# Performance work log

Hardware: AMD Instinct MI355X
Metric: run time of the kernel (lower is better)

The kernel has to match this reference:

```python
import jax, jax.numpy as jnp
import numpy as np

B, M, K, L, E = 1024, 16, 32, 50, 64
NUM_ACT, NUM_USER = 100000, 500000
AVG_M = float(M)  # avg group size; equals M since groups are batched to fixed size


def setup_inputs() -> dict:
    key = jax.random.key(0)
    ks = jax.random.split(key, 24)
    s = 1.0 / np.sqrt(E)
    u = lambda k, shape: jax.random.uniform(k, shape, minval=-s, maxval=s, dtype=jnp.float32)
    return {
        "members": jax.random.randint(ks[0], (B, M), 0, NUM_USER),
        "neighbors": jax.random.randint(ks[1], (B, M, K), 0, NUM_USER),
        "act_inputs": jax.random.randint(ks[2], (B,), 0, NUM_ACT),
        "act_seqs": jax.random.randint(ks[3], (B, M, L), 0, NUM_ACT),
        "act_table": jax.random.normal(ks[4], (NUM_ACT, E), dtype=jnp.float32) * 0.02,
        "user_table": jax.random.normal(ks[5], (NUM_USER, E), dtype=jnp.float32) * 0.02,
        "W_ih": u(ks[6], (4 * E, E)),
        "W_hh": u(ks[7], (4 * E, E)),
        "b_ih": u(ks[8], (4 * E,)),
        "b_hh": u(ks[9], (4 * E,)),
        "gcn_W": u(ks[10], (E, E)),
        "gcn_b": u(ks[11], (E,)),
        "pna_W1": u(ks[12], (4 * E, E)),
        "pna_b1": u(ks[13], (E,)),
        "pna_W2": u(ks[14], (E, E)),
        "pna_b2": u(ks[15], (E,)),
        "pna_W3": u(ks[16], (E, E)),
        "pna_b3": u(ks[17], (E,)),
        "pred_W1": u(ks[18], (3 * E, 8)),
        "pred_b1": u(ks[19], (8,)),
        "pred_W2": u(ks[20], (8, 1)),
        "pred_b2": u(ks[21], (1,)),
    }


def _lstm_last(x, W_ih, W_hh, b):
    # x: [N, L, E]; returns last hidden state [N, E] (PyTorch gate order i,f,g,o)
    n = x.shape[0]
    h0 = jnp.zeros((n, E), x.dtype)

    def step(carry, xt):
        h, c = carry
        gates = xt @ W_ih.T + h @ W_hh.T + b  # [N, 4E]
        i, f, g, o = jnp.split(gates, 4, axis=-1)
        c = jax.nn.sigmoid(f) * c + jax.nn.sigmoid(i) * jnp.tanh(g)
        h = jax.nn.sigmoid(o) * jnp.tanh(c)
        return (h, c), None

    (h, _), _ = jax.lax.scan(step, (h0, h0), jnp.swapaxes(x, 0, 1))
    return h


def reference(members, neighbors, act_inputs, act_seqs, act_table, user_table,
              W_ih, W_hh, b_ih, b_hh, gcn_W, gcn_b,
              pna_W1, pna_b1, pna_W2, pna_b2, pna_W3, pna_b3,
              pred_W1, pred_b1, pred_W2, pred_b2):
    act_e = act_table[act_inputs]  # [B, E] target activity embeddings
    # per-member LSTM encoding of activity sequences, batched over all B*M members
    seq_e = act_table[act_seqs].reshape(B * M, L, E)
    m_act = _lstm_last(seq_e, W_ih, W_hh, b_ih + b_hh).reshape(B, M, E)
    # GCN: mean over {member} U neighbors, then linear + relu
    mem_e = user_table[members]                     # [B, M, E]
    nbr_sum = user_table[neighbors].sum(axis=2)     # [B, M, E]
    agg = (mem_e + nbr_sum) / (K + 1)
    m_gcn = jax.nn.relu(agg @ gcn_W.T + gcn_b)      # [B, M, E]
    fus = m_act + m_gcn                             # [B, M, E]
    # PNA-style set aggregation: {mean,max} x {identity, amplification}
    mean = fus.mean(axis=1)
    mx = fus.max(axis=1)
    amp = jnp.log(M + 1.0) / jnp.log(AVG_M + 1.0)
    feats = jnp.concatenate([mean, mx, mean * amp, mx * amp], axis=-1)  # [B, 4E]
    h = jax.nn.relu(feats @ pna_W1 + pna_b1)
    h = jax.nn.relu(h @ pna_W2 + pna_b2)
    grp = h @ pna_W3 + pna_b3                        # [B, E]
    # predict layer
    cat = jnp.concatenate([grp * act_e, grp, act_e], axis=-1)  # [B, 3E]
    hh = jax.nn.relu(cat @ pred_W1 + pred_b1)
    y = jax.nn.sigmoid(hh @ pred_W2 + pred_b2)       # [B, 1]
    return y
```

## Files before the change

kernel.cpp:

```cpp
#include <hip/hip_runtime.h>
#include <hip/hip_bf16.h>
#include <math.h>

#define BB   1024
#define MM   16
#define KK   32
#define LL   50
#define EE   64
#define NACT 100000

typedef __attribute__((ext_vector_type(8))) short short8;
typedef float v4f __attribute__((ext_vector_type(4)));

__device__ __forceinline__ float rcpf(float x) { return __builtin_amdgcn_rcpf(x); }
__device__ __forceinline__ float exp2_fast(float x) {
    float r;
    asm("v_exp_f32 %0, %1" : "=v"(r) : "v"(x));
    return r;
}

__device__ __forceinline__ unsigned cvt_pk_bf16(float lo, float hi) {
    unsigned r;
    asm("v_cvt_pk_bf16_f32 %0, %1, %2" : "=v"(r) : "v"(lo), "v"(hi));
    return r;
}

__device__ __forceinline__ void block_sync_lds() {
    __builtin_amdgcn_sched_barrier(0);
    asm volatile("s_waitcnt lgkmcnt(0)" ::: "memory");
    __builtin_amdgcn_s_barrier();
    __builtin_amdgcn_sched_barrier(0);
}

__global__ __launch_bounds__(256)
void cvt_table(const float* __restrict__ src, unsigned* __restrict__ dst)
{
    const int i = blockIdx.x * 256 + threadIdx.x;
    if (i < (NACT * EE) / 8) {
        const float4* s = reinterpret_cast<const float4*>(src) + (size_t)i * 2;
        float4 a = s[0], b = s[1];
        uint4 o;
        o.x = cvt_pk_bf16(a.x, a.y);
        o.y = cvt_pk_bf16(a.z, a.w);
        o.z = cvt_pk_bf16(b.x, b.y);
        o.w = cvt_pk_bf16(b.z, b.w);
        reinterpret_cast<uint4*>(dst)[i] = o;
    }
}

__global__ __launch_bounds__(256, 2)
void lstm_fused(const int* __restrict__ act_seqs, const unsigned short* __restrict__ act_bf,
                const int* __restrict__ members, const int* __restrict__ neighbors,
                const float* __restrict__ user_table,
                const float* __restrict__ W_ih, const float* __restrict__ W_hh,
                const float* __restrict__ b_ih, const float* __restrict__ b_hh,
                const int* __restrict__ act_inputs, const float* __restrict__ act_table,
                const float* __restrict__ gcn_W, const float* __restrict__ gcn_b,
                const float* __restrict__ pna_W1, const float* __restrict__ pna_b1,
                const float* __restrict__ pna_W2, const float* __restrict__ pna_b2,
                const float* __restrict__ pna_W3, const float* __restrict__ pna_b3,
                const float* __restrict__ pred_W1, const float* __restrict__ pred_b1,
                const float* __restrict__ pred_W2, const float* __restrict__ pred_b2,
                float* __restrict__ out)
{
    __shared__ __align__(16) short sH[4][1024];
    __shared__ int sIdx[32 * LL];
    __shared__ int sNbr[32 * 33];
    __shared__ float sFus[32][66];
    __shared__ float sF[2][256];
    __shared__ float sP[2][2][64];
    __shared__ float sP7[2][8][8];
    __shared__ float sH1[2][64];
    __shared__ float sH2[2][64];
    __shared__ float sGrp[2][64];
    __shared__ float sActe[2][64];
    __shared__ float sHH[2][8];

    const int t    = threadIdx.x;
    const int blk  = blockIdx.x;
    const int lane = t & 63;
    const int w    = t >> 6;
    const int lr   = lane & 15;
    const int lb   = lane >> 4;

    for (int i = t; i < 32 * LL; i += 256) sIdx[i] = act_seqs[blk * (32 * LL) + i];
    for (int i = t; i < 32 * 33; i += 256) {
        const int p = i / 33, j = i - p * 33;
        const int base = blk * 32 + p;
        sNbr[i] = (j == 0) ? members[base] : neighbors[base * KK + j - 1];
    }
    if (t < 128) {
        const int q = t >> 6, e = t & 63;
        sActe[q][e] = act_table[(size_t)act_inputs[blk * 2 + q] * EE + e];
    }

    const float L2E = 1.44269504088896f;
    float gscale[4];
    gscale[0] = -L2E; gscale[1] = -L2E; gscale[2] = 2.0f * L2E; gscale[3] = -L2E;

    short8 Bf[2][4][2];
    #pragma unroll
    for (int mat = 0; mat < 2; ++mat) {
        const float* W = mat ? W_hh : W_ih;
        #pragma unroll
        for (int g = 0; g < 4; ++g) {
            const int j = g * 64 + w * 16 + lr;
            const float sc = gscale[g];
            #pragma unroll
            for (int ks = 0; ks < 2; ++ks) {
                const float4* p = reinterpret_cast<const float4*>(&W[(size_t)j * 64 + ks * 32 + lb * 8]);
                float4 v0 = p[0], v1 = p[1];
                uint4 o;
                o.x = cvt_pk_bf16(sc * v0.x, sc * v0.y);
                o.y = cvt_pk_bf16(sc * v0.z, sc * v0.w);
                o.z = cvt_pk_bf16(sc * v1.x, sc * v1.y);
                o.w = cvt_pk_bf16(sc * v1.z, sc * v1.w);
                Bf[mat][g][ks] = __builtin_bit_cast(short8, o);
            }
        }
    }
    short8 Bg[2];
    #pragma unroll
    for (int ks = 0; ks < 2; ++ks) {
        const int j = w * 16 + lr;
        const float4* p = reinterpret_cast<const float4*>(&gcn_W[(size_t)j * 64 + ks * 32 + lb * 8]);
        float4 v0 = p[0], v1 = p[1];
        uint4 o;
        o.x = cvt_pk_bf16(v0.x, v0.y);
        o.y = cvt_pk_bf16(v0.z, v0.w);
        o.z = cvt_pk_bf16(v1.x, v1.y);
        o.w = cvt_pk_bf16(v1.z, v1.w);
        Bg[ks] = __builtin_bit_cast(short8, o);
    }
    const float gb = gcn_b[w * 16 + lr];

    float bias[4];
    #pragma unroll
    for (int g = 0; g < 4; ++g) {
        const int j = g * 64 + w * 16 + lr;
        bias[g] = gscale[g] * (b_ih[j] + b_hh[j]);
    }

    float hA[4], cA[4], hB[4], cB[4];
    #pragma unroll
    for (int r = 0; r < 4; ++r) { hA[r] = 0.0f; cA[r] = 0.0f; hB[r] = 0.0f; cB[r] = 0.0f; }

    reinterpret_cast<uint4*>(sH)[t] = make_uint4(0u, 0u, 0u, 0u);
    __syncthreads();

    const int gpair = t >> 3;
    const int gec   = t & 7;
    const float* gut = user_table + (size_t)gec * 8;
    float gacc[8];
    #pragma unroll
    for (int q = 0; q < 8; ++q) gacc[q] = 0.0f;
    float4 gld0, gld1;
    {
        const int gi = sNbr[gpair * 33 + 0];
        const float4* gp = reinterpret_cast<const float4*>(gut + (size_t)gi * EE);
        gld0 = gp[0]; gld1 = gp[1];
    }

    const char* tbl8 = reinterpret_cast<const char*>(act_bf) + lb * 16;
    const int ibA = lr * LL;
    const int ibB = (16 + lr) * LL;

    int idA = sIdx[ibA + 0], idB = sIdx[ibB + 0];
    short8 axA0 = *reinterpret_cast<const short8*>(tbl8 + (size_t)idA * 128);
    short8 axA1 = *reinterpret_cast<const short8*>(tbl8 + (size_t)idA * 128 + 64);
    short8 axB0 = *reinterpret_cast<const short8*>(tbl8 + (size_t)idB * 128);
    short8 axB1 = *reinterpret_cast<const short8*>(tbl8 + (size_t)idB * 128 + 64);
    idA = sIdx[ibA + 1]; idB = sIdx[ibB + 1];

    const int offA0 = lr * 128 + ((lb ^ (lr & 7)) << 4);
    const int offA1 = lr * 128 + (((lb + 4) ^ (lr & 7)) << 4);
    int hw_off[4];
    #pragma unroll
    for (int r = 0; r < 4; ++r) {
        const int s = lb * 4 + r, e = w * 16 + lr;
        hw_off[r] = s * 128 + ((((e >> 3) ^ (s & 7)) << 4)) + (e & 7) * 2;
    }
    char* const sHb = reinterpret_cast<char*>(sH);

    #pragma unroll 2
    for (int step = 0; step < LL; ++step) {
        const int cb  = (step & 1) << 12;
        const int nb_ = cb ^ 4096;

        if (step < 33) {
            gacc[0] += gld0.x; gacc[1] += gld0.y; gacc[2] += gld0.z; gacc[3] += gld0.w;
            gacc[4] += gld1.x; gacc[5] += gld1.y; gacc[6] += gld1.z; gacc[7] += gld1.w;
            if (step < 32) {
                const int gi = sNbr[gpair * 33 + step + 1];
                const float4* gp = reinterpret_cast<const float4*>(gut + (size_t)gi * EE);
                gld0 = gp[0]; gld1 = gp[1];
            }
        }

        short8 nxA0 = *reinterpret_cast<const short8*>(tbl8 + (size_t)idA * 128);
        short8 nxA1 = *reinterpret_cast<const short8*>(tbl8 + (size_t)idA * 128 + 64);
        short8 nxB0 = *reinterpret_cast<const short8*>(tbl8 + (size_t)idB * 128);
        short8 nxB1 = *reinterpret_cast<const short8*>(tbl8 + (size_t)idB * 128 + 64);
        {
            const int s2 = (step + 2 < LL) ? (step + 2) : (LL - 1);
            idA = sIdx[ibA + s2]; idB = sIdx[ibB + s2];
        }

        short8 ahA0 = *reinterpret_cast<const short8*>(sHb + cb + offA0);
        short8 ahA1 = *reinterpret_cast<const short8*>(sHb + cb + offA1);
        short8 ahB0 = *reinterpret_cast<const short8*>(sHb + cb + 2048 + offA0);
        short8 ahB1 = *reinterpret_cast<const short8*>(sHb + cb + 2048 + offA1);

        v4f accA[4], accB[4];
        #pragma unroll
        for (int g = 0; g < 4; ++g) {
            v4f a; a[0] = bias[g]; a[1] = bias[g]; a[2] = bias[g]; a[3] = bias[g];
            accA[g] = a; accB[g] = a;
        }
        #pragma unroll
        for (int g = 0; g < 4; ++g) {
            accA[g] = __builtin_amdgcn_mfma_f32_16x16x32_bf16(axA0, Bf[0][g][0], accA[g], 0, 0, 0);
            accA[g] = __builtin_amdgcn_mfma_f32_16x16x32_bf16(axA1, Bf[0][g][1], accA[g], 0, 0, 0);
            accA[g] = __builtin_amdgcn_mfma_f32_16x16x32_bf16(ahA0, Bf[1][g][0], accA[g], 0, 0, 0);
            accA[g] = __builtin_amdgcn_mfma_f32_16x16x32_bf16(ahA1, Bf[1][g][1], accA[g], 0, 0, 0);
        }
        #pragma unroll
        for (int g = 0; g < 4; ++g) {
            accB[g] = __builtin_amdgcn_mfma_f32_16x16x32_bf16(axB0, Bf[0][g][0], accB[g], 0, 0, 0);
            accB[g] = __builtin_amdgcn_mfma_f32_16x16x32_bf16(axB1, Bf[0][g][1], accB[g], 0, 0, 0);
            accB[g] = __builtin_amdgcn_mfma_f32_16x16x32_bf16(ahB0, Bf[1][g][0], accB[g], 0, 0, 0);
            accB[g] = __builtin_amdgcn_mfma_f32_16x16x32_bf16(ahB1, Bf[1][g][1], accB[g], 0, 0, 0);
        }

        {
            char* SH = sHb + nb_;
            #pragma unroll
            for (int r = 0; r < 4; ++r) {
                const float si = rcpf(1.0f + exp2_fast(accA[0][r]));
                const float sf = rcpf(1.0f + exp2_fast(accA[1][r]));
                const float tg = fmaf(-2.0f, rcpf(1.0f + exp2_fast(accA[2][r])), 1.0f);
                const float so = rcpf(1.0f + exp2_fast(accA[3][r]));
                const float cc = fmaf(sf, cA[r], si * tg);
                cA[r] = cc;
                hA[r] = so * fmaf(-2.0f, rcpf(1.0f + exp2_fast(cc * (2.0f * L2E))), 1.0f);
            }
            const unsigned a01 = cvt_pk_bf16(hA[0], hA[1]);
            const unsigned a23 = cvt_pk_bf16(hA[2], hA[3]);
            *reinterpret_cast<short*>(SH + hw_off[0]) = (short)(a01 & 0xFFFF);
            *reinterpret_cast<short*>(SH + hw_off[1]) = (short)(a01 >> 16);
            *reinterpret_cast<short*>(SH + hw_off[2]) = (short)(a23 & 0xFFFF);
            *reinterpret_cast<short*>(SH + hw_off[3]) = (short)(a23 >> 16);
            SH += 2048;
            #pragma unroll
            for (int r = 0; r < 4; ++r) {
                const float si = rcpf(1.0f + exp2_fast(accB[0][r]));
                const float sf = rcpf(1.0f + exp2_fast(accB[1][r]));
                const float tg = fmaf(-2.0f, rcpf(1.0f + exp2_fast(accB[2][r])), 1.0f);
                const float so = rcpf(1.0f + exp2_fast(accB[3][r]));
                const float cc = fmaf(sf, cB[r], si * tg);
                cB[r] = cc;
                hB[r] = so * fmaf(-2.0f, rcpf(1.0f + exp2_fast(cc * (2.0f * L2E))), 1.0f);
            }
            const unsigned b01 = cvt_pk_bf16(hB[0], hB[1]);
            const unsigned b23 = cvt_pk_bf16(hB[2], hB[3]);
            *reinterpret_cast<short*>(SH + hw_off[0]) = (short)(b01 & 0xFFFF);
            *reinterpret_cast<short*>(SH + hw_off[1]) = (short)(b01 >> 16);
            *reinterpret_cast<short*>(SH + hw_off[2]) = (short)(b23 & 0xFFFF);
            *reinterpret_cast<short*>(SH + hw_off[3]) = (short)(b23 >> 16);
        }

        block_sync_lds();

        axA0 = nxA0; axA1 = nxA1; axB0 = nxB0; axB1 = nxB1;
    }


    {
        const float sc = 1.0f / 33.0f;
        uint4 pk;
        pk.x = cvt_pk_bf16(gacc[0] * sc, gacc[1] * sc);
        pk.y = cvt_pk_bf16(gacc[2] * sc, gacc[3] * sc);
        pk.z = cvt_pk_bf16(gacc[4] * sc, gacc[5] * sc);
        pk.w = cvt_pk_bf16(gacc[6] * sc, gacc[7] * sc);
        const int row = gpair & 15;
        const int off = ((gpair >> 4) << 11) + row * 128 + ((gec ^ (row & 7)) << 4);
        *reinterpret_cast<uint4*>(sHb + off) = pk;
    }
    __syncthreads();

    {
        short8 agA0 = *reinterpret_cast<const short8*>(sHb + offA0);
        short8 agA1 = *reinterpret_cast<const short8*>(sHb + offA1);
        short8 agB0 = *reinterpret_cast<const short8*>(sHb + 2048 + offA0);
        short8 agB1 = *reinterpret_cast<const short8*>(sHb + 2048 + offA1);
        v4f z4 = {0.0f, 0.0f, 0.0f, 0.0f};
        v4f gA = __builtin_amdgcn_mfma_f32_16x16x32_bf16(agA0, Bg[0], z4, 0, 0, 0);
        gA = __builtin_amdgcn_mfma_f32_16x16x32_bf16(agA1, Bg[1], gA, 0, 0, 0);
        v4f gB = __builtin_amdgcn_mfma_f32_16x16x32_bf16(agB0, Bg[0], z4, 0, 0, 0);
        gB = __builtin_amdgcn_mfma_f32_16x16x32_bf16(agB1, Bg[1], gB, 0, 0, 0);
        const int e = w * 16 + lr;
        #pragma unroll
        for (int r = 0; r < 4; ++r) {
            sFus[lb * 4 + r][e]      = hA[r] + fmaxf(gA[r] + gb, 0.0f);
            sFus[16 + lb * 4 + r][e] = hB[r] + fmaxf(gB[r] + gb, 0.0f);
        }
    }
    __syncthreads();

    if (t < 128) {
        const int q = t >> 6, e = t & 63;
        float mn = 0.0f, mx = -INFINITY;
        #pragma unroll
        for (int m = 0; m < MM; ++m) { float v = sFus[q * 16 + m][e]; mn += v; mx = fmaxf(mx, v); }
        mn *= (1.0f / 16.0f);
        sF[q][e] = mn; sF[q][64 + e] = mx; sF[q][128 + e] = mn; sF[q][192 + e] = mx;
    }
    __syncthreads();

    {
        const int q = t >> 7, kh = (t >> 6) & 1, j = t & 63;
        float p = 0.0f;
        const float* Wp = pna_W1 + (size_t)(kh * 128) * 64 + j;
        const float* fp = &sF[q][kh * 128];
        #pragma unroll 16
        for (int k = 0; k < 128; ++k) p = fmaf(fp[k], Wp[(size_t)k * 64], p);
        sP[q][kh][j] = p;
    }
    __syncthreads();
    if (t < 128) {
        const int q = t >> 6, j = t & 63;
        sH1[q][j] = fmaxf(pna_b1[j] + sP[q][0][j] + sP[q][1][j], 0.0f);
    }
    __syncthreads();

    {
        const int q = t >> 7, kh = (t >> 6) & 1, j = t & 63;
        float p = 0.0f;
        #pragma unroll
        for (int k = 0; k < 32; ++k)
            p = fmaf(sH1[q][kh * 32 + k], pna_W2[(size_t)(kh * 32 + k) * 64 + j], p);
        sP[q][kh][j] = p;
    }
    __syncthreads();
    if (t < 128) {
        const int q = t >> 6, j = t & 63;
        sH2[q][j] = fmaxf(pna_b2[j] + sP[q][0][j] + sP[q][1][j], 0.0f);
    }
    __syncthreads();

    {
        const int q = t >> 7, kh = (t >> 6) & 1, j = t & 63;
        float p = 0.0f;
        #pragma unroll
        for (int k = 0; k < 32; ++k)
            p = fmaf(sH2[q][kh * 32 + k], pna_W3[(size_t)(kh * 32 + k) * 64 + j], p);
        sP[q][kh][j] = p;
    }
    __syncthreads();
    if (t < 128) {
        const int q = t >> 6, j = t & 63;
        sGrp[q][j] = pna_b3[j] + sP[q][0][j] + sP[q][1][j];
    }
    __syncthreads();

    if (t < 128) {
        const int q = t >> 6, kg = (t >> 3) & 7, j = t & 7;
        float a = 0.0f;
        #pragma unroll
        for (int kk = 0; kk < 24; ++kk) {
            const int k = kg * 24 + kk;
            const float cv = (k < 64) ? sGrp[q][k] * sActe[q][k]
                                      : ((k < 128) ? sGrp[q][k - 64] : sActe[q][k - 128]);
            a = fmaf(cv, pred_W1[k * 8 + j], a);
        }
        sP7[q][kg][j] = a;
    }
    __syncthreads();
    if (t < 16) {
        const int q = t >> 3, j = t & 7;
        float a = pred_b1[j];
        #pragma unroll
        for (int kg = 0; kg < 8; ++kg) a += sP7[q][kg][j];
        sHH[q][j] = fmaxf(a, 0.0f);
    }
    __syncthreads();
    if (t < 2) {
        float y = pred_b2[0];
        #pragma unroll
        for (int jj = 0; jj < 8; ++jj) y = fmaf(sHH[t][jj], pred_W2[jj], y);
        out[blk * 2 + t] = 1.0f / (1.0f + expf(-y));
    }
}

extern "C" void kernel_launch(void* const* d_in, const int* in_sizes, int n_in,
                              void* d_out, int out_size, void* d_ws, size_t ws_size,
                              hipStream_t stream) {
    const int*   members    = (const int*)d_in[0];
    const int*   neighbors  = (const int*)d_in[1];
    const int*   act_inputs = (const int*)d_in[2];
    const int*   act_seqs   = (const int*)d_in[3];
    const float* act_table  = (const float*)d_in[4];
    const float* user_table = (const float*)d_in[5];
    const float* W_ih       = (const float*)d_in[6];
    const float* W_hh       = (const float*)d_in[7];
    const float* b_ih       = (const float*)d_in[8];
    const float* b_hh       = (const float*)d_in[9];
    const float* gcn_W      = (const float*)d_in[10];
    const float* gcn_b      = (const float*)d_in[11];
    const float* pna_W1     = (const float*)d_in[12];
    const float* pna_b1     = (const float*)d_in[13];
    const float* pna_W2     = (const float*)d_in[14];
    const float* pna_b2     = (const float*)d_in[15];
    const float* pna_W3     = (const float*)d_in[16];
    const float* pna_b3     = (const float*)d_in[17];
    const float* pred_W1    = (const float*)d_in[18];
    const float* pred_b1    = (const float*)d_in[19];
    const float* pred_W2    = (const float*)d_in[20];
    const float* pred_b2    = (const float*)d_in[21];

    unsigned short* act_bf = (unsigned short*)d_ws;

    cvt_table<<<dim3((NACT * EE / 8 + 255) / 256), dim3(256), 0, stream>>>(
        act_table, (unsigned*)act_bf);

    lstm_fused<<<dim3(512), dim3(256), 0, stream>>>(
        act_seqs, act_bf, members, neighbors, user_table,
        W_ih, W_hh, b_ih, b_hh,
        act_inputs, act_table,
        gcn_W, gcn_b, pna_W1, pna_b1, pna_W2, pna_b2, pna_W3, pna_b3,
        pred_W1, pred_b1, pred_W2, pred_b2, (float*)d_out);
}
```

Baseline: 106.0 us.

## Precompute next-step input projection MFMAs before barrier to shorten recurrent critical path

```diff
diff --git a/kernel.cpp b/kernel.cpp
--- a/kernel.cpp
+++ b/kernel.cpp
@@ -166,11 +166,27 @@
     const int ibB = (16 + lr) * LL;
 
     int idA = sIdx[ibA + 0], idB = sIdx[ibB + 0];
-    short8 axA0 = *reinterpret_cast<const short8*>(tbl8 + (size_t)idA * 128);
-    short8 axA1 = *reinterpret_cast<const short8*>(tbl8 + (size_t)idA * 128 + 64);
-    short8 axB0 = *reinterpret_cast<const short8*>(tbl8 + (size_t)idB * 128);
-    short8 axB1 = *reinterpret_cast<const short8*>(tbl8 + (size_t)idB * 128 + 64);
+    short8 c0A0 = *reinterpret_cast<const short8*>(tbl8 + (size_t)idA * 128);
+    short8 c0A1 = *reinterpret_cast<const short8*>(tbl8 + (size_t)idA * 128 + 64);
+    short8 c0B0 = *reinterpret_cast<const short8*>(tbl8 + (size_t)idB * 128);
+    short8 c0B1 = *reinterpret_cast<const short8*>(tbl8 + (size_t)idB * 128 + 64);
     idA = sIdx[ibA + 1]; idB = sIdx[ibB + 1];
+    short8 pxA0 = *reinterpret_cast<const short8*>(tbl8 + (size_t)idA * 128);
+    short8 pxA1 = *reinterpret_cast<const short8*>(tbl8 + (size_t)idA * 128 + 64);
+    short8 pxB0 = *reinterpret_cast<const short8*>(tbl8 + (size_t)idB * 128);
+    short8 pxB1 = *reinterpret_cast<const short8*>(tbl8 + (size_t)idB * 128 + 64);
+    idA = sIdx[ibA + 2]; idB = sIdx[ibB + 2];
+
+    v4f xaccA[4], xaccB[4];
+    #pragma unroll
+    for (int g = 0; g < 4; ++g) {
+        v4f a; a[0] = bias[g]; a[1] = bias[g]; a[2] = bias[g]; a[3] = bias[g];
+        a = __builtin_amdgcn_mfma_f32_16x16x32_bf16(c0A0, Bf[0][g][0], a, 0, 0, 0);
+        xaccA[g] = __builtin_amdgcn_mfma_f32_16x16x32_bf16(c0A1, Bf[0][g][1], a, 0, 0, 0);
+        v4f b; b[0] = bias[g]; b[1] = bias[g]; b[2] = bias[g]; b[3] = bias[g];
+        b = __builtin_amdgcn_mfma_f32_16x16x32_bf16(c0B0, Bf[0][g][0], b, 0, 0, 0);
+        xaccB[g] = __builtin_amdgcn_mfma_f32_16x16x32_bf16(c0B1, Bf[0][g][1], b, 0, 0, 0);
+    }
 
     const int offA0 = lr * 128 + ((lb ^ (lr & 7)) << 4);
     const int offA1 = lr * 128 + (((lb + 4) ^ (lr & 7)) << 4);
@@ -202,7 +218,7 @@
         short8 nxB0 = *reinterpret_cast<const short8*>(tbl8 + (size_t)idB * 128);
         short8 nxB1 = *reinterpret_cast<const short8*>(tbl8 + (size_t)idB * 128 + 64);
         {
-            const int s2 = (step + 2 < LL) ? (step + 2) : (LL - 1);
+            const int s2 = (step + 3 < LL) ? (step + 3) : (LL - 1);
             idA = sIdx[ibA + s2]; idB = sIdx[ibB + s2];
         }
 
@@ -214,22 +230,10 @@
         v4f accA[4], accB[4];
         #pragma unroll
         for (int g = 0; g < 4; ++g) {
-            v4f a; a[0] = bias[g]; a[1] = bias[g]; a[2] = bias[g]; a[3] = bias[g];
-            accA[g] = a; accB[g] = a;
-        }
-        #pragma unroll
-        for (int g = 0; g < 4; ++g) {
-            accA[g] = __builtin_amdgcn_mfma_f32_16x16x32_bf16(axA0, Bf[0][g][0], accA[g], 0, 0, 0);
-            accA[g] = __builtin_amdgcn_mfma_f32_16x16x32_bf16(axA1, Bf[0][g][1], accA[g], 0, 0, 0);
-            accA[g] = __builtin_amdgcn_mfma_f32_16x16x32_bf16(ahA0, Bf[1][g][0], accA[g], 0, 0, 0);
-            accA[g] = __builtin_amdgcn_mfma_f32_16x16x32_bf16(ahA1, Bf[1][g][1], accA[g], 0, 0, 0);
-        }
-        #pragma unroll
-        for (int g = 0; g < 4; ++g) {
-            accB[g] = __builtin_amdgcn_mfma_f32_16x16x32_bf16(axB0, Bf[0][g][0], accB[g], 0, 0, 0);
-            accB[g] = __builtin_amdgcn_mfma_f32_16x16x32_bf16(axB1, Bf[0][g][1], accB[g], 0, 0, 0);
-            accB[g] = __builtin_amdgcn_mfma_f32_16x16x32_bf16(ahB0, Bf[1][g][0], accB[g], 0, 0, 0);
-            accB[g] = __builtin_amdgcn_mfma_f32_16x16x32_bf16(ahB1, Bf[1][g][1], accB[g], 0, 0, 0);
+            v4f a = __builtin_amdgcn_mfma_f32_16x16x32_bf16(ahA0, Bf[1][g][0], xaccA[g], 0, 0, 0);
+            accA[g] = __builtin_amdgcn_mfma_f32_16x16x32_bf16(ahA1, Bf[1][g][1], a, 0, 0, 0);
+            v4f b = __builtin_amdgcn_mfma_f32_16x16x32_bf16(ahB0, Bf[1][g][0], xaccB[g], 0, 0, 0);
+            accB[g] = __builtin_amdgcn_mfma_f32_16x16x32_bf16(ahB1, Bf[1][g][1], b, 0, 0, 0);
         }
 
         {
@@ -269,9 +273,19 @@
             *reinterpret_cast<short*>(SH + hw_off[3]) = (short)(b23 >> 16);
         }
 
+        #pragma unroll
+        for (int g = 0; g < 4; ++g) {
+            v4f a; a[0] = bias[g]; a[1] = bias[g]; a[2] = bias[g]; a[3] = bias[g];
+            a = __builtin_amdgcn_mfma_f32_16x16x32_bf16(pxA0, Bf[0][g][0], a, 0, 0, 0);
+            xaccA[g] = __builtin_amdgcn_mfma_f32_16x16x32_bf16(pxA1, Bf[0][g][1], a, 0, 0, 0);
+            v4f b; b[0] = bias[g]; b[1] = bias[g]; b[2] = bias[g]; b[3] = bias[g];
+            b = __builtin_amdgcn_mfma_f32_16x16x32_bf16(pxB0, Bf[0][g][0], b, 0, 0, 0);
+            xaccB[g] = __builtin_amdgcn_mfma_f32_16x16x32_bf16(pxB1, Bf[0][g][1], b, 0, 0, 0);
+        }
+
         block_sync_lds();
 
-        axA0 = nxA0; axA1 = nxA1; axB0 = nxB0; axB1 = nxB1;
+        pxA0 = nxA0; pxA1 = nxA1; pxB0 = nxB0; pxB1 = nxB1;
     }
 
 
```

Result: no change. 105.1 us (-0.8%).
